# Kernel optimization log

Hardware: AMD Instinct MI355X
Metric: run time of the kernel (lower is better)

The kernel has to match this reference:

```python
import jax, jax.numpy as jnp
import numpy as np

B, F, E, U = 16384, 1024, 8, 512
EH1, EH2 = 1024, 1024
TH1, TH2 = 512, 256
T = 4


def setup_inputs() -> dict:
    key = jax.random.key(0)
    ks = jax.random.split(key, 16)
    s = lambda k, shape: jax.random.normal(k, shape, dtype=jnp.float32) * 0.02
    return {
        "x": jax.random.normal(ks[0], (B, F), dtype=jnp.float32),
        # stacked expert MLP params [E, ...]
        "We1": s(ks[1], (E, F, EH1)), "be1": s(ks[2], (E, EH1)),
        "We2": s(ks[3], (E, EH1, EH2)), "be2": s(ks[4], (E, EH2)),
        "We3": s(ks[5], (E, EH2, U)), "be3": s(ks[6], (E, U)),
        # per-task gates [T, F, E]
        "Wg": jax.random.normal(ks[7], (T, F, E), dtype=jnp.float32),
        # stacked tower params [T, ...]
        "Wt1": s(ks[8], (T, U, TH1)), "bt1": s(ks[9], (T, TH1)),
        "Wt2": s(ks[10], (T, TH1, TH2)), "bt2": s(ks[11], (T, TH2)),
        "Wt3": s(ks[12], (T, TH2, 1)), "bt3": s(ks[13], (T, 1)),
    }


def reference(x, We1, be1, We2, be2, We3, be3, Wg, Wt1, bt1, Wt2, bt2, Wt3, bt3):
    relu = jax.nn.relu
    # experts: all E small MLPs batched as one grouped GEMM chain -> [E, B, U]
    h = relu(jnp.einsum('bf,efh->ebh', x, We1) + be1[:, None, :])
    h = relu(jnp.einsum('ebh,ehk->ebk', h, We2) + be2[:, None, :])
    expert_out = jnp.einsum('ebk,eku->ebu', h, We3) + be3[:, None, :]
    # per-task gates: softmax over expert axis -> [T, B, E]
    gates = jax.nn.softmax(jnp.einsum('bf,tfe->tbe', x, Wg), axis=-1)
    # gate-weighted combine over experts -> [T, B, U]
    ti = jnp.einsum('tbe,ebu->tbu', gates, expert_out)
    # per-task towers -> [T, B, 1]
    g = relu(jnp.einsum('tbu,tuh->tbh', ti, Wt1) + bt1[:, None, :])
    g = relu(jnp.einsum('tbh,thk->tbk', g, Wt2) + bt2[:, None, :])
    out = jnp.einsum('tbk,tko->tbo', g, Wt3) + bt3[:, None, :]
    return out  # [T, B, 1], equivalent to list of per-task [B, 1] outputs
```

## Files before the change

kernel.cpp:

```cpp
#include <hip/hip_runtime.h>
#include <hip/hip_bf16.h>
#include <cstdint>

#define B_ 16384
#define F_ 1024
#define E_ 8
#define U_ 512
#define EH1_ 1024
#define EH2_ 1024
#define TH1_ 512
#define TH2_ 256
#define T_ 4

typedef __attribute__((ext_vector_type(4))) float f32x4;
typedef __attribute__((ext_vector_type(8))) short bf16x8;
typedef __attribute__((ext_vector_type(4))) short s16x4;

__device__ __forceinline__ short f2bf(float f) {
  union { float f; unsigned u; } v; v.f = f;
  unsigned r = v.u + 0x7fffu + ((v.u >> 16) & 1u);
  return (short)(r >> 16);
}
__device__ __forceinline__ float bf2f(short s) {
  union { unsigned u; float f; } v; v.u = ((unsigned)(unsigned short)s) << 16;
  return v.f;
}

__device__ __forceinline__ void gload16(const void* g, void* l) {
  __builtin_amdgcn_global_load_lds(
      (const __attribute__((address_space(1))) void*)g,
      (__attribute__((address_space(3))) void*)l, 16, 0, 0);
}

__global__ __launch_bounds__(256) void conv_dual(const float* __restrict__ in,
                                                 short* __restrict__ ob,
                                                 short* __restrict__ orr, long n) {
  long i = ((long)blockIdx.x * 256 + threadIdx.x) * 8;
  if (i >= n) return;
  const float4* p = (const float4*)(in + i);
  float4 a = p[0], b = p[1];
  float v[8] = {a.x, a.y, a.z, a.w, b.x, b.y, b.z, b.w};
  bf16x8 o, r;
#pragma unroll
  for (int j = 0; j < 8; j++) {
    short s = f2bf(v[j]);
    o[j] = s;
    r[j] = f2bf(v[j] - bf2f(s));
  }
  *(bf16x8*)(ob + i) = o;
  *(bf16x8*)(orr + i) = r;
}

__global__ __launch_bounds__(256) void trans_conv(const float* __restrict__ W,
                                                  short* __restrict__ Wt, int K, int N) {
  __shared__ float tile[32][33];
  const int e = blockIdx.z;
  const int k0 = blockIdx.x * 32, n0 = blockIdx.y * 32;
  const float* We = W + (size_t)e * K * N;
  short* Wte = Wt + (size_t)e * N * K;
  const int tx = threadIdx.x, ty = threadIdx.y;
#pragma unroll
  for (int r = 0; r < 32; r += 8)
    tile[ty + r][tx] = We[(size_t)(k0 + ty + r) * N + (n0 + tx)];
  __syncthreads();
#pragma unroll
  for (int r = 0; r < 32; r += 8)
    Wte[(size_t)(n0 + ty + r) * K + (k0 + tx)] = f2bf(tile[tx][ty + r]);
}

__global__ __launch_bounds__(256) void trans_wg(const float* __restrict__ Wg,
                                                short* __restrict__ Wp,
                                                short* __restrict__ Wr) {
  int idx = blockIdx.x * 256 + threadIdx.x;
  int p = idx >> 10, f = idx & 1023;
  int t = p >> 3, e = p & 7;
  float w = Wg[((size_t)t * F_ + f) * E_ + e];
  short wb = f2bf(w);
  Wp[idx] = wb;
  Wr[idx] = f2bf(w - bf2f(wb));
}

__global__ __launch_bounds__(256) void glogits(const short* __restrict__ xb,
                                               const short* __restrict__ xr,
                                               const short* __restrict__ Wp,
                                               const short* __restrict__ Wr,
                                               float* __restrict__ gates) {
  const int wid = threadIdx.x >> 6, lane = threadIdx.x & 63;
  const int m0 = blockIdx.x * 64 + wid * 16;
  const int fr = lane & 15, kg = (lane >> 4) * 8;
  f32x4 acc[2];
#pragma unroll
  for (int j = 0; j < 2; j++)
#pragma unroll
    for (int r = 0; r < 4; r++) acc[j][r] = 0.f;

  const short* Aterm[3] = {xb, xb, xr};
  const short* Bterm[3] = {Wp, Wr, Wp};
#pragma unroll
  for (int term = 0; term < 3; ++term) {
    const short* A = Aterm[term] + (size_t)(m0 + fr) * F_ + kg;
    const short* Bt0 = Bterm[term] + (size_t)fr * F_ + kg;
    const short* Bt1 = Bterm[term] + (size_t)(16 + fr) * F_ + kg;
    for (int k0 = 0; k0 < F_; k0 += 32) {
      bf16x8 a = *(const bf16x8*)(A + k0);
      bf16x8 b0 = *(const bf16x8*)(Bt0 + k0);
      bf16x8 b1 = *(const bf16x8*)(Bt1 + k0);
      acc[0] = __builtin_amdgcn_mfma_f32_16x16x32_bf16(a, b0, acc[0], 0, 0, 0);
      acc[1] = __builtin_amdgcn_mfma_f32_16x16x32_bf16(a, b1, acc[1], 0, 0, 0);
    }
  }
  const int cc = lane & 15;
#pragma unroll
  for (int j = 0; j < 2; ++j) {
    const int t = j * 2 + (cc >> 3), e = cc & 7;
#pragma unroll
    for (int r = 0; r < 4; ++r) {
      float s = acc[j][r];
      float mx = s;
      mx = fmaxf(mx, __shfl_xor(mx, 1, 64));
      mx = fmaxf(mx, __shfl_xor(mx, 2, 64));
      mx = fmaxf(mx, __shfl_xor(mx, 4, 64));
      float ex = __expf(s - mx);
      float sm = ex;
      sm += __shfl_xor(sm, 1, 64);
      sm += __shfl_xor(sm, 2, 64);
      sm += __shfl_xor(sm, 4, 64);
      const int b = m0 + (lane >> 4) * 4 + r;
      gates[((size_t)t * B_ + b) * E_ + e] = ex / sm;
    }
  }
}

template <int RELU>
__global__ __launch_bounds__(256, 2) void gemm_bt(const short* __restrict__ A0, size_t sA,
                                                  const short* __restrict__ B0, size_t sB,
                                                  const float* __restrict__ bias0, size_t sBias,
                                                  short* __restrict__ C0, size_t sC,
                                                  int M, int N, int K) {
  const int z = blockIdx.z;
  const short* A = A0 + (size_t)z * sA;
  const short* Bt = B0 + (size_t)z * sB;
  const float* bias = bias0 + (size_t)z * sBias;
  short* C = C0 + (size_t)z * sC;

  __shared__ short As[128 * 32];
  __shared__ short Bs[128 * 32];
  const int tid = threadIdx.x;
  const int wid = tid >> 6;
  const int lane = tid & 63;
  const int m0 = blockIdx.x * 128;
  const int n0 = blockIdx.y * 128;
  const int wm = (wid >> 1) * 64;
  const int wn = (wid & 1) * 64;

  f32x4 acc[4][4];
#pragma unroll
  for (int i = 0; i < 4; i++)
#pragma unroll
    for (int j = 0; j < 4; j++)
#pragma unroll
      for (int r = 0; r < 4; r++) acc[i][j][r] = 0.f;

  const int srow = wid * 16 + (lane >> 2);
  const int scol = (lane & 3) * 8;
  const short* aSrc = A + (size_t)(m0 + srow) * K + scol;
  const short* bSrc = Bt + (size_t)(n0 + srow) * K + scol;
  short* aDst = As + wid * 512;
  short* bDst = Bs + wid * 512;
  const size_t halfoff = (size_t)64 * K;

  const int fr = lane & 15;
  const int kg = (lane >> 4) * 8;

  for (int k0 = 0; k0 < K; k0 += 32) {
    gload16(aSrc + k0, aDst);
    gload16(aSrc + halfoff + k0, aDst + 2048);
    gload16(bSrc + k0, bDst);
    gload16(bSrc + halfoff + k0, bDst + 2048);
    __syncthreads();
    bf16x8 af[4], bfv[4];
#pragma unroll
    for (int i = 0; i < 4; i++) af[i] = *(const bf16x8*)&As[(wm + i * 16 + fr) * 32 + kg];
#pragma unroll
    for (int j = 0; j < 4; j++) bfv[j] = *(const bf16x8*)&Bs[(wn + j * 16 + fr) * 32 + kg];
#pragma unroll
    for (int i = 0; i < 4; i++)
#pragma unroll
      for (int j = 0; j < 4; j++)
        acc[i][j] = __builtin_amdgcn_mfma_f32_16x16x32_bf16(af[i], bfv[j], acc[i][j], 0, 0, 0);
    __syncthreads();
  }

  const int cr4 = (lane >> 4) * 4;
  const int cc = lane & 15;
#pragma unroll
  for (int j = 0; j < 4; j++) {
    const int col = n0 + wn + j * 16 + cc;
    const float bv = bias[col];
#pragma unroll
    for (int i = 0; i < 4; i++) {
      const int row = m0 + wm + i * 16 + cr4;
#pragma unroll
      for (int r = 0; r < 4; r++) {
        float v = acc[i][j][r] + bv;
        if (RELU) v = fmaxf(v, 0.f);
        C[(size_t)(row + r) * N + col] = f2bf(v);
      }
    }
  }
}

__global__ __launch_bounds__(256) void combine_kernel(const short* __restrict__ EO,
                                                      const float* __restrict__ gates,
                                                      short* __restrict__ ti,
                                                      int Bc, int b0) {
  const int idx = blockIdx.x * 256 + threadIdx.x;
  const int lb = idx >> 6;
  const int uc = (idx & 63) * 8;
  float acc[T_][8];
#pragma unroll
  for (int t = 0; t < T_; t++)
#pragma unroll
    for (int j = 0; j < 8; j++) acc[t][j] = 0.f;
#pragma unroll
  for (int e = 0; e < E_; e++) {
    bf16x8 v = *(const bf16x8*)&EO[((size_t)e * Bc + lb) * U_ + uc];
    float f[8];
#pragma unroll
    for (int j = 0; j < 8; j++) f[j] = bf2f(v[j]);
#pragma unroll
    for (int t = 0; t < T_; t++) {
      const float g = gates[((size_t)t * B_ + b0 + lb) * E_ + e];
#pragma unroll
      for (int j = 0; j < 8; j++) acc[t][j] += g * f[j];
    }
  }
#pragma unroll
  for (int t = 0; t < T_; t++) {
    bf16x8 o;
#pragma unroll
    for (int j = 0; j < 8; j++) o[j] = f2bf(acc[t][j]);
    *(bf16x8*)&ti[((size_t)t * Bc + lb) * U_ + uc] = o;
  }
}

__global__ __launch_bounds__(256) void tower3_kernel(const short* __restrict__ G2,
                                                     const float* __restrict__ Wt3,
                                                     const float* __restrict__ bt3,
                                                     float* __restrict__ out,
                                                     int bcShift, int b0) {
  const int wid = threadIdx.x >> 6, lane = threadIdx.x & 63;
  const int rowl = blockIdx.x * 4 + wid;
  const int t = rowl >> bcShift;
  const int lb = rowl & ((1 << bcShift) - 1);
  const short* g = G2 + (size_t)rowl * TH2_;
  s16x4 gv = *(const s16x4*)(g + lane * 4);
  float4 wv = *(const float4*)(Wt3 + t * TH2_ + lane * 4);
  float s = bf2f(gv[0]) * wv.x + bf2f(gv[1]) * wv.y + bf2f(gv[2]) * wv.z + bf2f(gv[3]) * wv.w;
#pragma unroll
  for (int off = 32; off; off >>= 1) s += __shfl_xor(s, off, 64);
  if (lane == 0) out[(size_t)t * B_ + b0 + lb] = s + bt3[t];
}

extern "C" void kernel_launch(void* const* d_in, const int* in_sizes, int n_in,
                              void* d_out, int out_size, void* d_ws, size_t ws_size,
                              hipStream_t stream) {
  const float* x   = (const float*)d_in[0];
  const float* We1 = (const float*)d_in[1];
  const float* be1 = (const float*)d_in[2];
  const float* We2 = (const float*)d_in[3];
  const float* be2 = (const float*)d_in[4];
  const float* We3 = (const float*)d_in[5];
  const float* be3 = (const float*)d_in[6];
  const float* Wg  = (const float*)d_in[7];
  const float* Wt1 = (const float*)d_in[8];
  const float* bt1 = (const float*)d_in[9];
  const float* Wt2 = (const float*)d_in[10];
  const float* bt2 = (const float*)d_in[11];
  const float* Wt3 = (const float*)d_in[12];
  const float* bt3 = (const float*)d_in[13];
  float* out = (float*)d_out;
  (void)in_sizes; (void)n_in; (void)out_size;

  char* ws = (char*)d_ws;
  size_t off = 0;
  auto alloc = [&](size_t bytes) {
    char* p = ws + off;
    off += (bytes + 255) & ~(size_t)255;
    return p;
  };
  short* We1b  = (short*)alloc((size_t)E_ * F_ * EH1_ * 2);
  short* We2b  = (short*)alloc((size_t)E_ * EH1_ * EH2_ * 2);
  short* We3b  = (short*)alloc((size_t)E_ * EH2_ * U_ * 2);
  short* Wt1b  = (short*)alloc((size_t)T_ * U_ * TH1_ * 2);
  short* Wt2b  = (short*)alloc((size_t)T_ * TH1_ * TH2_ * 2);
  short* Wgp   = (short*)alloc((size_t)32 * F_ * 2);
  short* Wgr   = (short*)alloc((size_t)32 * F_ * 2);
  float* gates = (float*)alloc((size_t)T_ * B_ * E_ * 4);
  short* xb    = (short*)alloc((size_t)B_ * F_ * 2);
  short* xrb   = (short*)alloc((size_t)B_ * F_ * 2);
  const size_t persist = off;

  int Bc = 16384;
  while (Bc > 256 && persist + (size_t)Bc * 36864 + 65536 > ws_size) Bc >>= 1;
  const int bcShift = __builtin_ctz((unsigned)Bc);

  short* h1 = (short*)alloc((size_t)E_ * Bc * EH1_ * 2);
  short* h2 = (short*)alloc((size_t)E_ * Bc * EH2_ * 2);
  short* ti = (short*)alloc((size_t)T_ * Bc * U_ * 2);
  short* EO = h1;
  short* G1 = h2;
  short* G2 = h2 + (size_t)T_ * Bc * TH1_;

  conv_dual<<<(B_ * F_ / 8 + 255) / 256, 256, 0, stream>>>(x, xb, xrb, (long)B_ * F_);
  dim3 tb(32, 8);
  trans_conv<<<dim3(F_ / 32, EH1_ / 32, E_), tb, 0, stream>>>(We1, We1b, F_, EH1_);
  trans_conv<<<dim3(EH1_ / 32, EH2_ / 32, E_), tb, 0, stream>>>(We2, We2b, EH1_, EH2_);
  trans_conv<<<dim3(EH2_ / 32, U_ / 32, E_), tb, 0, stream>>>(We3, We3b, EH2_, U_);
  trans_conv<<<dim3(U_ / 32, TH1_ / 32, T_), tb, 0, stream>>>(Wt1, Wt1b, U_, TH1_);
  trans_conv<<<dim3(TH1_ / 32, TH2_ / 32, T_), tb, 0, stream>>>(Wt2, Wt2b, TH1_, TH2_);
  trans_wg<<<(32 * F_) / 256, 256, 0, stream>>>(Wg, Wgp, Wgr);

  glogits<<<B_ / 64, 256, 0, stream>>>(xb, xrb, Wgp, Wgr, gates);

  for (int b0 = 0; b0 < B_; b0 += Bc) {
    const short* xc = xb + (size_t)b0 * F_;
    gemm_bt<1><<<dim3(Bc / 128, EH1_ / 128, E_), 256, 0, stream>>>(
        xc, 0, We1b, (size_t)F_ * EH1_, be1, EH1_, h1, (size_t)Bc * EH1_, Bc, EH1_, F_);
    gemm_bt<1><<<dim3(Bc / 128, EH2_ / 128, E_), 256, 0, stream>>>(
        h1, (size_t)Bc * EH1_, We2b, (size_t)EH1_ * EH2_, be2, EH2_, h2, (size_t)Bc * EH2_,
        Bc, EH2_, EH1_);
    gemm_bt<0><<<dim3(Bc / 128, U_ / 128, E_), 256, 0, stream>>>(
        h2, (size_t)Bc * EH2_, We3b, (size_t)EH2_ * U_, be3, U_, EO, (size_t)Bc * U_,
        Bc, U_, EH2_);
    combine_kernel<<<(Bc * 64) / 256, 256, 0, stream>>>(EO, gates, ti, Bc, b0);
    gemm_bt<1><<<dim3(Bc / 128, TH1_ / 128, T_), 256, 0, stream>>>(
        ti, (size_t)Bc * U_, Wt1b, (size_t)U_ * TH1_, bt1, TH1_, G1, (size_t)Bc * TH1_,
        Bc, TH1_, U_);
    gemm_bt<1><<<dim3(Bc / 128, TH2_ / 128, T_), 256, 0, stream>>>(
        G1, (size_t)Bc * TH1_, Wt2b, (size_t)TH1_ * TH2_, bt2, TH2_, G2, (size_t)Bc * TH2_,
        Bc, TH2_, TH1_);
    tower3_kernel<<<T_ * Bc / 4, 256, 0, stream>>>(G2, Wt3, bt3, out, bcShift, b0);
  }
}
```

Baseline: 1.145 ms.

## Add 256x256-tile pipelined bf16 GEMM for expert layers

Adds a new GEMM kernel that uses 256x256 output tiles with 512 threads, 128KB of swizzled LDS holding double-buffered A and B slabs, and interleaved global-to-LDS prefetch with MFMA compute. It raises s_setprio around the MFMA blocks. The three expert GEMMs switch to this kernel, while the tower GEMMs keep the old 128x128 kernel. The larger tiles are meant to raise arithmetic intensity and hide load latency, at the cost of fewer blocks per layer and higher register and LDS pressure, which may limit occupancy.

Result: no change. 1.165 ms (+1.8%).

```diff
diff --git a/kernel.cpp b/kernel.cpp
--- a/kernel.cpp
+++ b/kernel.cpp
@@ -127,6 +127,152 @@
       sm += __shfl_xor(sm, 4, 64);
       const int b = m0 + (lane >> 4) * 4 + r;
       gates[((size_t)t * B_ + b) * E_ + e] = ex / sm;
+    }
+  }
+}
+
+template <int RELU>
+__global__ __launch_bounds__(512, 2) void gemm256(const short* __restrict__ A0, size_t sA,
+                                                  const short* __restrict__ B0, size_t sB,
+                                                  const float* __restrict__ bias0, size_t sBias,
+                                                  short* __restrict__ C0, size_t sC,
+                                                  int M, int N, int K) {
+  const int z = blockIdx.z;
+  const short* A = A0 + (size_t)z * sA;
+  const short* Bt = B0 + (size_t)z * sB;
+  const float* bias = bias0 + (size_t)z * sBias;
+  short* C = C0 + (size_t)z * sC;
+
+  __shared__ short lds[65536];
+  const int tid = threadIdx.x;
+  const int wid = tid >> 6, lane = tid & 63;
+  const int wr = wid >> 2, wc = wid & 3;
+  const int m0g = blockIdx.x * 256, n0g = blockIdx.y * 256;
+  const int lrow = lane & 15;
+  const int kgb = (lane >> 4) * 16;
+  const int NT = K >> 6;
+
+  f32x4 acc[8][4];
+#pragma unroll
+  for (int m = 0; m < 8; m++)
+#pragma unroll
+    for (int n = 0; n < 4; n++)
+#pragma unroll
+      for (int r = 0; r < 4; r++) acc[m][n][r] = 0.f;
+
+  auto stage = [&](int slabSh, const short* Mat, int row0, int kcolSh) {
+#pragma unroll
+    for (int c = 0; c < 2; ++c) {
+      int X = c * 8192 + tid * 16;
+      int row = X >> 6;
+      int swz = ((row ^ (row >> 2)) & 3) << 4;
+      int colb = (X & 63) ^ swz;
+      const short* src = Mat + (size_t)(row0 + row) * (size_t)K + kcolSh + (colb >> 1);
+      gload16(src, &lds[slabSh + c * 4096 + (wid << 9)]);
+    }
+  };
+  auto rdA = [&](int slabSh, int m) -> bf16x8 {
+    int row = wr * 128 + m * 16 + lrow;
+    int swz = ((row ^ (row >> 2)) & 3) << 4;
+    return *(const bf16x8*)&lds[slabSh + row * 32 + ((kgb ^ swz) >> 1)];
+  };
+  auto rdB = [&](int slabSh, int n) -> bf16x8 {
+    int row = wc * 64 + n * 16 + lrow;
+    int swz = ((row ^ (row >> 2)) & 3) << 4;
+    return *(const bf16x8*)&lds[slabSh + row * 32 + ((kgb ^ swz) >> 1)];
+  };
+
+  stage(32768, Bt, n0g, 0);
+  stage(0, A, m0g, 0);
+  stage(49152, Bt, n0g, 32);
+  stage(16384, A, m0g, 32);
+  stage(32768 + 8192, Bt, n0g, 64);
+  stage(0 + 8192, A, m0g, 64);
+  stage(49152 + 8192, Bt, n0g, 96);
+  asm volatile("s_waitcnt vmcnt(6)" ::: "memory");
+  __builtin_amdgcn_s_barrier();
+
+  for (int tau = 0; tau < NT; ++tau) {
+    const int bs = (tau & 1) * 8192;
+    const int nbs = ((tau + 1) & 1) * 8192;
+    bf16x8 Bf[4], Af[4];
+
+#pragma unroll
+    for (int n = 0; n < 4; ++n) Bf[n] = rdB(32768 + bs, n);
+#pragma unroll
+    for (int m = 0; m < 4; ++m) Af[m] = rdA(bs, m);
+    if (tau + 1 < NT) stage(16384 + nbs, A, m0g, (tau + 1) * 64 + 32);
+    __builtin_amdgcn_s_barrier();
+    __builtin_amdgcn_s_setprio(1);
+#pragma unroll
+    for (int m = 0; m < 4; ++m)
+#pragma unroll
+      for (int n = 0; n < 4; ++n)
+        acc[m][n] = __builtin_amdgcn_mfma_f32_16x16x32_bf16(Af[m], Bf[n], acc[m][n], 0, 0, 0);
+    __builtin_amdgcn_s_setprio(0);
+    __builtin_amdgcn_s_barrier();
+
+#pragma unroll
+    for (int m = 0; m < 4; ++m) Af[m] = rdA(bs, 4 + m);
+    if (tau + 2 < NT) stage(32768 + bs, Bt, n0g, (tau + 2) * 64);
+    __builtin_amdgcn_s_barrier();
+    __builtin_amdgcn_s_setprio(1);
+#pragma unroll
+    for (int m = 0; m < 4; ++m)
+#pragma unroll
+      for (int n = 0; n < 4; ++n)
+        acc[4 + m][n] = __builtin_amdgcn_mfma_f32_16x16x32_bf16(Af[m], Bf[n], acc[4 + m][n], 0, 0, 0);
+    __builtin_amdgcn_s_setprio(0);
+    __builtin_amdgcn_s_barrier();
+
+#pragma unroll
+    for (int n = 0; n < 4; ++n) Bf[n] = rdB(49152 + bs, n);
+#pragma unroll
+    for (int m = 0; m < 4; ++m) Af[m] = rdA(16384 + bs, m);
+    if (tau + 2 < NT) stage(bs, A, m0g, (tau + 2) * 64);
+    __builtin_amdgcn_s_barrier();
+    __builtin_amdgcn_s_setprio(1);
+#pragma unroll
+    for (int m = 0; m < 4; ++m)
+#pragma unroll
+      for (int n = 0; n < 4; ++n)
+        acc[m][n] = __builtin_amdgcn_mfma_f32_16x16x32_bf16(Af[m], Bf[n], acc[m][n], 0, 0, 0);
+    __builtin_amdgcn_s_setprio(0);
+    __builtin_amdgcn_s_barrier();
+
+#pragma unroll
+    for (int m = 0; m < 4; ++m) Af[m] = rdA(16384 + bs, 4 + m);
+    if (tau + 2 < NT) stage(49152 + bs, Bt, n0g, (tau + 2) * 64 + 32);
+    __builtin_amdgcn_s_barrier();
+    __builtin_amdgcn_s_setprio(1);
+#pragma unroll
+    for (int m = 0; m < 4; ++m)
+#pragma unroll
+      for (int n = 0; n < 4; ++n)
+        acc[4 + m][n] = __builtin_amdgcn_mfma_f32_16x16x32_bf16(Af[m], Bf[n], acc[4 + m][n], 0, 0, 0);
+    __builtin_amdgcn_s_setprio(0);
+    if (tau < NT - 2)
+      asm volatile("s_waitcnt vmcnt(6)" ::: "memory");
+    else if (tau == NT - 2)
+      asm volatile("s_waitcnt vmcnt(0)" ::: "memory");
+    __builtin_amdgcn_s_barrier();
+  }
+
+  const int cr4 = (lane >> 4) * 4;
+  const int cc = lane & 15;
+#pragma unroll
+  for (int j = 0; j < 4; ++j) {
+    const int col = n0g + wc * 64 + j * 16 + cc;
+    const float bv = bias[col];
+#pragma unroll
+    for (int m = 0; m < 8; ++m) {
+      const int row = m0g + wr * 128 + m * 16 + cr4;
+#pragma unroll
+      for (int r = 0; r < 4; ++r) {
+        float v = acc[m][j][r] + bv;
+        if (RELU) v = fmaxf(v, 0.f);
+        C[(size_t)(row + r) * N + col] = f2bf(v);
+      }
     }
   }
 }
@@ -325,12 +471,12 @@
 
   for (int b0 = 0; b0 < B_; b0 += Bc) {
     const short* xc = xb + (size_t)b0 * F_;
-    gemm_bt<1><<<dim3(Bc / 128, EH1_ / 128, E_), 256, 0, stream>>>(
+    gemm256<1><<<dim3(Bc / 256, EH1_ / 256, E_), 512, 0, stream>>>(
         xc, 0, We1b, (size_t)F_ * EH1_, be1, EH1_, h1, (size_t)Bc * EH1_, Bc, EH1_, F_);
-    gemm_bt<1><<<dim3(Bc / 128, EH2_ / 128, E_), 256, 0, stream>>>(
+    gemm256<1><<<dim3(Bc / 256, EH2_ / 256, E_), 512, 0, stream>>>(
         h1, (size_t)Bc * EH1_, We2b, (size_t)EH1_ * EH2_, be2, EH2_, h2, (size_t)Bc * EH2_,
         Bc, EH2_, EH1_);
-    gemm_bt<0><<<dim3(Bc / 128, U_ / 128, E_), 256, 0, stream>>>(
+    gemm256<0><<<dim3(Bc / 256, U_ / 256, E_), 512, 0, stream>>>(
         h2, (size_t)Bc * EH2_, We3b, (size_t)EH2_ * U_, be3, U_, EO, (size_t)Bc * U_,
         Bc, U_, EH2_);
     combine_kernel<<<(Bc * 64) / 256, 256, 0, stream>>>(EO, gates, ti, Bc, b0);
```

## Process two K-slices per barrier in GEMM and shrink workspace by aliasing ti into h2

Applied to the files above, without the earlier changes.

The GEMM main loop now loads two 32-wide K slices into separate LDS buffers per iteration, halving the number of __syncthreads barriers per K. It also raises wave priority around the MFMA bursts. The workspace is reorganized so ti, G1 and G2 all alias into h2, which lowers per-row memory and may let a larger batch chunk fit. The trade-off is double the LDS use per block, which could reduce occupancy.

Result: faster. 1.032 ms (-9.9%).

```diff
diff --git a/kernel.cpp b/kernel.cpp
--- a/kernel.cpp
+++ b/kernel.cpp
@@ -143,8 +143,8 @@
   const float* bias = bias0 + (size_t)z * sBias;
   short* C = C0 + (size_t)z * sC;
 
-  __shared__ short As[128 * 32];
-  __shared__ short Bs[128 * 32];
+  __shared__ short As0[128 * 32], As1[128 * 32];
+  __shared__ short Bs0[128 * 32], Bs1[128 * 32];
   const int tid = threadIdx.x;
   const int wid = tid >> 6;
   const int lane = tid & 63;
@@ -161,33 +161,54 @@
 #pragma unroll
       for (int r = 0; r < 4; r++) acc[i][j][r] = 0.f;
 
-  const int srow = wid * 16 + (lane >> 2);
-  const int scol = (lane & 3) * 8;
-  const short* aSrc = A + (size_t)(m0 + srow) * K + scol;
-  const short* bSrc = Bt + (size_t)(n0 + srow) * K + scol;
-  short* aDst = As + wid * 512;
-  short* bDst = Bs + wid * 512;
-  const size_t halfoff = (size_t)64 * K;
+  const int srow = tid >> 2;
+  const int scol = (tid & 3) * 8;
+  const short* aS = A + (size_t)(m0 + srow) * K + scol;
+  const short* bS = Bt + (size_t)(n0 + srow) * K + scol;
+  const size_t r64 = (size_t)64 * K;
+  const int wds = wid << 9;
 
   const int fr = lane & 15;
   const int kg = (lane >> 4) * 8;
 
-  for (int k0 = 0; k0 < K; k0 += 32) {
-    gload16(aSrc + k0, aDst);
-    gload16(aSrc + halfoff + k0, aDst + 2048);
-    gload16(bSrc + k0, bDst);
-    gload16(bSrc + halfoff + k0, bDst + 2048);
+  for (int k0 = 0; k0 < K; k0 += 64) {
+    gload16(aS + k0, As0 + wds);
+    gload16(aS + r64 + k0, As0 + 2048 + wds);
+    gload16(aS + k0 + 32, As1 + wds);
+    gload16(aS + r64 + k0 + 32, As1 + 2048 + wds);
+    gload16(bS + k0, Bs0 + wds);
+    gload16(bS + r64 + k0, Bs0 + 2048 + wds);
+    gload16(bS + k0 + 32, Bs1 + wds);
+    gload16(bS + r64 + k0 + 32, Bs1 + 2048 + wds);
     __syncthreads();
-    bf16x8 af[4], bfv[4];
-#pragma unroll
-    for (int i = 0; i < 4; i++) af[i] = *(const bf16x8*)&As[(wm + i * 16 + fr) * 32 + kg];
-#pragma unroll
-    for (int j = 0; j < 4; j++) bfv[j] = *(const bf16x8*)&Bs[(wn + j * 16 + fr) * 32 + kg];
-#pragma unroll
-    for (int i = 0; i < 4; i++)
-#pragma unroll
-      for (int j = 0; j < 4; j++)
-        acc[i][j] = __builtin_amdgcn_mfma_f32_16x16x32_bf16(af[i], bfv[j], acc[i][j], 0, 0, 0);
+    {
+      bf16x8 af[4], bfv[4];
+#pragma unroll
+      for (int i = 0; i < 4; i++) af[i] = *(const bf16x8*)&As0[(wm + i * 16 + fr) * 32 + kg];
+#pragma unroll
+      for (int j = 0; j < 4; j++) bfv[j] = *(const bf16x8*)&Bs0[(wn + j * 16 + fr) * 32 + kg];
+      __builtin_amdgcn_s_setprio(1);
+#pragma unroll
+      for (int i = 0; i < 4; i++)
+#pragma unroll
+        for (int j = 0; j < 4; j++)
+          acc[i][j] = __builtin_amdgcn_mfma_f32_16x16x32_bf16(af[i], bfv[j], acc[i][j], 0, 0, 0);
+      __builtin_amdgcn_s_setprio(0);
+    }
+    {
+      bf16x8 af[4], bfv[4];
+#pragma unroll
+      for (int i = 0; i < 4; i++) af[i] = *(const bf16x8*)&As1[(wm + i * 16 + fr) * 32 + kg];
+#pragma unroll
+      for (int j = 0; j < 4; j++) bfv[j] = *(const bf16x8*)&Bs1[(wn + j * 16 + fr) * 32 + kg];
+      __builtin_amdgcn_s_setprio(1);
+#pragma unroll
+      for (int i = 0; i < 4; i++)
+#pragma unroll
+        for (int j = 0; j < 4; j++)
+          acc[i][j] = __builtin_amdgcn_mfma_f32_16x16x32_bf16(af[i], bfv[j], acc[i][j], 0, 0, 0);
+      __builtin_amdgcn_s_setprio(0);
+    }
     __syncthreads();
   }
 
@@ -302,15 +323,15 @@
   const size_t persist = off;
 
   int Bc = 16384;
-  while (Bc > 256 && persist + (size_t)Bc * 36864 + 65536 > ws_size) Bc >>= 1;
+  while (Bc > 256 && persist + (size_t)Bc * 32768 + 65536 > ws_size) Bc >>= 1;
   const int bcShift = __builtin_ctz((unsigned)Bc);
 
   short* h1 = (short*)alloc((size_t)E_ * Bc * EH1_ * 2);
   short* h2 = (short*)alloc((size_t)E_ * Bc * EH2_ * 2);
-  short* ti = (short*)alloc((size_t)T_ * Bc * U_ * 2);
   short* EO = h1;
-  short* G1 = h2;
-  short* G2 = h2 + (size_t)T_ * Bc * TH1_;
+  short* ti = h2;
+  short* G1 = h2 + (size_t)Bc * 2048;
+  short* G2 = h2 + (size_t)Bc * 4096;
 
   conv_dual<<<(B_ * F_ / 8 + 255) / 256, 256, 0, stream>>>(x, xb, xrb, (long)B_ * F_);
   dim3 tb(32, 8);
```
